# Kernel tuning notes

Measured on AMD Instinct MI355X. Metric: run time of the kernel, lower is better.

Reference implementation:

```python
import math
import jax, jax.numpy as jnp
import numpy as np

B, S, HID, H, NREL = 4, 512, 1024, 16, 64
D = HID // H  # per-head size = 64, must equal relation embedding dim


def setup_inputs() -> dict:
    key = jax.random.key(0)
    ks = jax.random.split(key, 12)
    w = lambda k, shape: jax.random.normal(k, shape, jnp.float32) * 0.02
    return {
        "q_in": jax.random.normal(ks[0], (B, S, HID), jnp.float32),
        "k_in": jax.random.normal(ks[1], (B, S, HID), jnp.float32),
        "v_in": jax.random.normal(ks[2], (B, S, HID), jnp.float32),
        "mask": jax.random.randint(ks[3], (B, 1, S, S), 0, NREL),
        "Wq": w(ks[4], (HID, HID)), "bq": jnp.zeros((HID,), jnp.float32),
        "Wk": w(ks[5], (HID, HID)), "bk": jnp.zeros((HID,), jnp.float32),
        "Wv": w(ks[6], (HID, HID)), "bv": jnp.zeros((HID,), jnp.float32),
        "Wo": w(ks[7], (HID, HID)), "bo": jnp.zeros((HID,), jnp.float32),
        "rel_k_table": w(ks[8], (NREL, D)),
        "rel_v_table": w(ks[9], (NREL, D)),
    }


def reference(q_in, k_in, v_in, mask, Wq, bq, Wk, bk, Wv, bv, Wo, bo,
              rel_k_table, rel_v_table):
    def proj(x, W, b):  # [B,S,HID] -> [B,H,S,D]
        return (x @ W.T + b).reshape(B, S, H, D).transpose(0, 2, 1, 3)

    q = proj(q_in, Wq, bq)
    k = proj(k_in, Wk, bk)
    v = proj(v_in, Wv, bv)

    ids = mask[:, 0]                      # [B,S,S] relation ids
    rel_k = rel_k_table[ids]              # [B,S,S,D]
    rel_v = rel_v_table[ids]              # [B,S,S,D]

    scores = jnp.einsum('bhqd,bhkd->bhqk', q, k)
    scores = scores + jnp.einsum('bhqd,bqkd->bhqk', q, rel_k) / 4.0
    scores = scores / math.sqrt(float(D))

    bias = (1.0 - (mask > 0).astype(scores.dtype)) * -10000.0  # [B,1,S,S]
    probs = jax.nn.softmax(scores + bias, axis=-1)             # [B,H,S,S]

    out = jnp.einsum('bhqk,bhkd->bhqd', probs, v)
    out = out + 0.25 * jnp.einsum('bhqk,bqkd->bhqd', probs, rel_v)
    out = out.transpose(0, 2, 1, 3).reshape(B, S, HID)
    return out @ Wo.T + bo
```

## Files before the change

kernel.cpp:

```cpp
#include <hip/hip_runtime.h>


typedef __attribute__((ext_vector_type(8))) short bf16x8 __attribute__((may_alias));
typedef __attribute__((ext_vector_type(4))) float f32x4;

__device__ __forceinline__ short f2bf(float x) {
    unsigned u = __float_as_uint(x);
    u += 0x7fff + ((u >> 16) & 1);
    return (short)(u >> 16);
}

__device__ __forceinline__ void async16(void* lds, const void* g) {
    __builtin_amdgcn_global_load_lds(
        (const __attribute__((address_space(1))) void*)g,
        (__attribute__((address_space(3))) void*)lds, 16, 0, 0);
}

__global__ __launch_bounds__(256)
void cast_all(const float* __restrict__ x0, const float* __restrict__ x1, const float* __restrict__ x2,
              const float* __restrict__ w0, const float* __restrict__ w1,
              const float* __restrict__ w2, const float* __restrict__ w3,
              short* __restrict__ y0, short* __restrict__ y1, short* __restrict__ y2,
              short* __restrict__ u0, short* __restrict__ u1,
              short* __restrict__ u2, short* __restrict__ u3)
{
    size_t i = (size_t)blockIdx.x * 256 + threadIdx.x;
    const float* src; short* dst; size_t off;
    if (i < 3u*524288u) {
        int s = (int)(i / 524288u); off = i % 524288u;
        src = s == 0 ? x0 : (s == 1 ? x1 : x2);
        dst = s == 0 ? y0 : (s == 1 ? y1 : y2);
    } else {
        size_t j = i - 3u*524288u;
        int s = (int)(j / 262144u); off = j % 262144u;
        src = s == 0 ? w0 : (s == 1 ? w1 : (s == 2 ? w2 : w3));
        dst = s == 0 ? u0 : (s == 1 ? u1 : (s == 2 ? u2 : u3));
    }
    float4 f = ((const float4*)src)[off];
    short4 o; o.x = f2bf(f.x); o.y = f2bf(f.y); o.z = f2bf(f.z); o.w = f2bf(f.w);
    ((short4*)dst)[off] = o;
}

__global__ __launch_bounds__(256)
void gemm_bf16(const short* __restrict__ A0, const short* __restrict__ A1, const short* __restrict__ A2,
               const short* __restrict__ B0, const short* __restrict__ B1, const short* __restrict__ B2,
               const float* __restrict__ c0, const float* __restrict__ c1, const float* __restrict__ c2,
               void* __restrict__ O0, void* __restrict__ O1, void* __restrict__ O2,
               int mode)
{
    __shared__ short ldsw[128 * 64 + 64 * 64];
    short* Als = ldsw;
    short* Bls = ldsw + 128 * 64;

    const int z = blockIdx.z;
    const short* A    = z == 0 ? A0 : (z == 1 ? A1 : A2);
    const short* Bm   = z == 0 ? B0 : (z == 1 ? B1 : B2);
    const float* bias = z == 0 ? c0 : (z == 1 ? c1 : c2);
    void*        O    = z == 0 ? O0 : (z == 1 ? O1 : O2);

    const int t = threadIdx.x;
    const int lane = t & 63, w = t >> 6;
    const int rowBase = blockIdx.y * 128;
    const int colBase = blockIdx.x * 64;
    const int gl = ((lane & 7) - (lane >> 3)) & 7;

    f32x4 acc[2][4];
#pragma unroll
    for (int i = 0; i < 2; ++i)
#pragma unroll
        for (int j = 0; j < 4; ++j) acc[i][j] = (f32x4){0.f, 0.f, 0.f, 0.f};

    const int rstage = w * 8 + (lane >> 3);
    const short* Ag = A  + (size_t)(rowBase + rstage) * 1024 + gl * 8;
    const short* Bg = Bm + (size_t)(colBase + rstage) * 1024 + gl * 8;

    for (int it = 0; it < 16; ++it) {
        const int k0 = it * 64;
#pragma unroll
        for (int i = 0; i < 4; ++i)
            async16(&Als[(i * 32 + w * 8) * 64], Ag + (size_t)i * 32 * 1024 + k0);
#pragma unroll
        for (int i = 0; i < 2; ++i)
            async16(&Bls[(i * 32 + w * 8) * 64], Bg + (size_t)i * 32 * 1024 + k0);
        __syncthreads();
#pragma unroll
        for (int kk = 0; kk < 2; ++kk) {
            bf16x8 a[2], b[4];
#pragma unroll
            for (int mi = 0; mi < 2; ++mi) {
                int r = w * 32 + mi * 16 + (lane & 15);
                int s = (kk * 4 + (lane >> 4) + r) & 7;
                a[mi] = *(const bf16x8*)&Als[r * 64 + s * 8];
            }
#pragma unroll
            for (int ni = 0; ni < 4; ++ni) {
                int r = ni * 16 + (lane & 15);
                int s = (kk * 4 + (lane >> 4) + r) & 7;
                b[ni] = *(const bf16x8*)&Bls[r * 64 + s * 8];
            }
#pragma unroll
            for (int mi = 0; mi < 2; ++mi)
#pragma unroll
                for (int ni = 0; ni < 4; ++ni)
                    acc[mi][ni] = __builtin_amdgcn_mfma_f32_16x16x32_bf16(
                        a[mi], b[ni], acc[mi][ni], 0, 0, 0);
        }
        __syncthreads();
    }

    const int quad = lane >> 4, cl = lane & 15;
    if (mode == 1 && z == 2) {
        short* Tls = ldsw;
#pragma unroll
        for (int mi = 0; mi < 2; ++mi)
#pragma unroll
            for (int ni = 0; ni < 4; ++ni) {
                int d = ni * 16 + cl;
                float bv = bias[colBase + d];
                short4 pk;
                pk.x = f2bf(acc[mi][ni][0] + bv);
                pk.y = f2bf(acc[mi][ni][1] + bv);
                pk.z = f2bf(acc[mi][ni][2] + bv);
                pk.w = f2bf(acc[mi][ni][3] + bv);
                int sl = w * 32 + mi * 16 + quad * 4;
                *(short4*)&Tls[d * 136 + sl] = pk;
            }
        __syncthreads();
        int d = t >> 2, s0 = (t & 3) * 32;
        int bb = rowBase >> 9, hh = colBase >> 6, sBase = rowBase & 511;
        short* dst = (short*)O + (((size_t)(bb * 16 + hh) * 64 + d) << 9) + sBase + s0;
#pragma unroll
        for (int j = 0; j < 4; ++j)
            *(bf16x8*)(dst + j * 8) = *(const bf16x8*)&Tls[d * 136 + s0 + j * 8];
        return;
    }

#pragma unroll
    for (int mi = 0; mi < 2; ++mi) {
#pragma unroll
        for (int ni = 0; ni < 4; ++ni) {
            int col = colBase + ni * 16 + cl;
            float bv = bias[col];
#pragma unroll
            for (int reg = 0; reg < 4; ++reg) {
                int row = rowBase + w * 32 + mi * 16 + quad * 4 + reg;
                float val = acc[mi][ni][reg] + bv;
                if (mode == 1) {
                    int bb = row >> 9, s = row & 511;
                    int hh = col >> 6, d = col & 63;
                    ((short*)O)[(((size_t)(bb * 16 + hh) * 512 + s) << 6) + d] = f2bf(val);
                } else {
                    ((float*)O)[(size_t)row * 1024 + col] = val;
                }
            }
        }
    }
}

#define A_LDS_BINS 4160
#define A_LDS_OPP  21568
#define A_LDS_LP   38208
#define A_LDS_INV  38464
#define A_LDS_TOT  38528

__global__ __launch_bounds__(256)
void attn_kernel(const short* __restrict__ qg, const short* __restrict__ kg,
                 const short* __restrict__ vtg, const int* __restrict__ mask,
                 const float* __restrict__ relk, const float* __restrict__ relv,
                 short* __restrict__ attn_b)
{
    __shared__ __align__(16) char pool[A_LDS_TOT];
    float* qwr    = (float*)pool;
    short* binsBf = (short*)pool;
    float* binsA  = (float*)(pool + A_LDS_BINS);
    float* Lp     = (float*)(pool + A_LDS_LP);
    float* invl   = (float*)(pool + A_LDS_INV);

    const int t = threadIdx.x, lane = t & 63, w = t >> 6;
    const int quad = lane >> 4, cl = lane & 15;
    const int bid = blockIdx.x, qbk = bid & 31, bh = bid >> 5;
    const int b = bh >> 4, h = bh & 15, q0 = qbk * 16;

    const short* qbase = qg  + ((size_t)bh * 512 + q0) * 64;
    const short* kbase = kg  + (size_t)bh * 512 * 64;
    const short* vbase = vtg + (size_t)bh * 64 * 512;
    const int*   mb    = mask + (size_t)b * 512 * 512 + (size_t)q0 * 512;

    float* bins_w = binsA + w * (16 * 68);
    short* Pst    = (short*)(pool + A_LDS_OPP + w * 4160);
    float* Op_w   = (float*)(pool + A_LDS_OPP + w * 4160);

    for (int i = t; i < 4 * 16 * 68; i += 256) binsA[i] = 0.f;

    bf16x8 rvb0, rvb1;
    {
        const float* rp = relv + (size_t)(quad * 8) * 64 + w * 16 + cl;
#pragma unroll
        for (int j = 0; j < 8; ++j) rvb0[j] = f2bf(rp[j * 64]);
#pragma unroll
        for (int j = 0; j < 8; ++j) rvb1[j] = f2bf(rp[2048 + j * 64]);
    }

    bf16x8 qa0 = *(const bf16x8*)(qbase + cl * 64 + quad * 8);
    bf16x8 qa1 = *(const bf16x8*)(qbase + cl * 64 + 32 + quad * 8);

    {
        const float* kp = relk + (size_t)(w * 16 + cl) * 64 + quad * 8;
        bf16x8 rb0, rb1;
#pragma unroll
        for (int j = 0; j < 8; ++j) rb0[j] = f2bf(kp[j]);
#pragma unroll
        for (int j = 0; j < 8; ++j) rb1[j] = f2bf(kp[32 + j]);
        f32x4 qr = (f32x4){0.f, 0.f, 0.f, 0.f};
        qr = __builtin_amdgcn_mfma_f32_16x16x32_bf16(qa0, rb0, qr, 0, 0, 0);
        qr = __builtin_amdgcn_mfma_f32_16x16x32_bf16(qa1, rb1, qr, 0, 0, 0);
#pragma unroll
        for (int reg = 0; reg < 4; ++reg)
            qwr[(quad * 4 + reg) * 65 + w * 16 + cl] = qr[reg];
    }
    __syncthreads();

    f32x4 oacc[4];
#pragma unroll
    for (int dt = 0; dt < 4; ++dt) oacc[dt] = (f32x4){0.f, 0.f, 0.f, 0.f};
    float lpart[4] = {0.f, 0.f, 0.f, 0.f};

#pragma unroll
    for (int c = 0; c < 2; ++c) {
        const int k0 = w * 128 + c * 64;
#pragma unroll
        for (int nt = 0; nt < 4; ++nt) {
            const short* kp = kbase + (size_t)(k0 + nt * 16 + cl) * 64 + quad * 8;
            bf16x8 kb0 = *(const bf16x8*)kp;
            bf16x8 kb1 = *(const bf16x8*)(kp + 32);
            f32x4 s = (f32x4){0.f, 0.f, 0.f, 0.f};
            s = __builtin_amdgcn_mfma_f32_16x16x32_bf16(qa0, kb0, s, 0, 0, 0);
            s = __builtin_amdgcn_mfma_f32_16x16x32_bf16(qa1, kb1, s, 0, 0, 0);
            const int kidx = k0 + nt * 16 + cl;
#pragma unroll
            for (int reg = 0; reg < 4; ++reg) {
                int q = quad * 4 + reg;
                int id = mb[q * 512 + kidx];
                float sc = (s[reg] + 0.25f * qwr[q * 65 + id]) * 0.125f;
                sc = (id == 0) ? sc - 10000.f : sc;
                float p = __expf(sc);
                lpart[reg] += p;
                atomicAdd(&bins_w[q * 68 + id], p);
                Pst[q * 72 + nt * 16 + cl] = f2bf(p);
            }
        }
        bf16x8 pa0 = *(const bf16x8*)&Pst[cl * 72 + quad * 8];
        bf16x8 pa1 = *(const bf16x8*)&Pst[cl * 72 + 32 + quad * 8];
#pragma unroll
        for (int dt = 0; dt < 4; ++dt) {
            const short* vp = vbase + (size_t)(dt * 16 + cl) * 512 + k0 + quad * 8;
            bf16x8 vb0 = *(const bf16x8*)vp;
            bf16x8 vb1 = *(const bf16x8*)(vp + 32);
            oacc[dt] = __builtin_amdgcn_mfma_f32_16x16x32_bf16(pa0, vb0, oacc[dt], 0, 0, 0);
            oacc[dt] = __builtin_amdgcn_mfma_f32_16x16x32_bf16(pa1, vb1, oacc[dt], 0, 0, 0);
        }
    }

#pragma unroll
    for (int reg = 0; reg < 4; ++reg) {
        int q = quad * 4 + reg;
#pragma unroll
        for (int dt = 0; dt < 4; ++dt)
            Op_w[q * 65 + dt * 16 + cl] = oacc[dt][reg];
        float lsum = lpart[reg];
#pragma unroll
        for (int m = 8; m >= 1; m >>= 1) lsum += __shfl_xor(lsum, m);
        if (cl == 0) Lp[w * 16 + q] = lsum;
    }
    __syncthreads();

    if (t < 16)
        invl[t] = 1.0f / (Lp[t] + Lp[16 + t] + Lp[32 + t] + Lp[48 + t]);
    {
        int q = t >> 4, r0 = (t & 15) * 4;
        float4 s0 = *(const float4*)&binsA[0 * 1088 + q * 68 + r0];
        float4 s1 = *(const float4*)&binsA[1 * 1088 + q * 68 + r0];
        float4 s2 = *(const float4*)&binsA[2 * 1088 + q * 68 + r0];
        float4 s3 = *(const float4*)&binsA[3 * 1088 + q * 68 + r0];
        short4 o;
        o.x = f2bf(s0.x + s1.x + s2.x + s3.x);
        o.y = f2bf(s0.y + s1.y + s2.y + s3.y);
        o.z = f2bf(s0.z + s1.z + s2.z + s3.z);
        o.w = f2bf(s0.w + s1.w + s2.w + s3.w);
        *(short4*)&binsBf[q * 72 + r0] = o;
    }
    __syncthreads();

    bf16x8 ba0 = *(const bf16x8*)&binsBf[cl * 72 + quad * 8];
    bf16x8 ba1 = *(const bf16x8*)&binsBf[cl * 72 + 32 + quad * 8];
    f32x4 racc = (f32x4){0.f, 0.f, 0.f, 0.f};
    racc = __builtin_amdgcn_mfma_f32_16x16x32_bf16(ba0, rvb0, racc, 0, 0, 0);
    racc = __builtin_amdgcn_mfma_f32_16x16x32_bf16(ba1, rvb1, racc, 0, 0, 0);

#pragma unroll
    for (int reg = 0; reg < 4; ++reg) {
        int q = quad * 4 + reg;
        int d = w * 16 + cl;
        float osum = 0.f;
#pragma unroll
        for (int wv = 0; wv < 4; ++wv)
            osum += ((const float*)(pool + A_LDS_OPP + wv * 4160))[q * 65 + d];
        float val = (osum + 0.25f * racc[reg]) * invl[q];
        attn_b[(size_t)(b * 512 + q0 + q) * 1024 + h * 64 + d] = f2bf(val);
    }
}

extern "C" void kernel_launch(void* const* d_in, const int* in_sizes, int n_in,
                              void* d_out, int out_size, void* d_ws, size_t ws_size,
                              hipStream_t stream)
{
    const float* q_in = (const float*)d_in[0];
    const float* k_in = (const float*)d_in[1];
    const float* v_in = (const float*)d_in[2];
    const int*   mask = (const int*)d_in[3];
    const float* Wq   = (const float*)d_in[4];
    const float* bq   = (const float*)d_in[5];
    const float* Wk   = (const float*)d_in[6];
    const float* bk   = (const float*)d_in[7];
    const float* Wv   = (const float*)d_in[8];
    const float* bv   = (const float*)d_in[9];
    const float* Wo   = (const float*)d_in[10];
    const float* bo   = (const float*)d_in[11];
    const float* relk = (const float*)d_in[12];
    const float* relv = (const float*)d_in[13];

    char* ws = (char*)d_ws;
    short* qb     = (short*)(ws);
    short* kb     = (short*)(ws + (4u  << 20));
    short* vt     = (short*)(ws + (8u  << 20));
    short* attn_b = (short*)(ws + (12u << 20));
    short* Xq     = (short*)(ws + (16u << 20));
    short* Xk     = (short*)(ws + (20u << 20));
    short* Xv     = (short*)(ws + (24u << 20));
    short* Wqb    = (short*)(ws + (28u << 20));
    short* Wkb    = (short*)(ws + (30u << 20));
    short* Wvb    = (short*)(ws + (32u << 20));
    short* Wob    = (short*)(ws + (34u << 20));

    cast_all<<<10240, 256, 0, stream>>>(q_in, k_in, v_in, Wq, Wk, Wv, Wo,
                                        Xq, Xk, Xv, Wqb, Wkb, Wvb, Wob);

    gemm_bf16<<<dim3(16, 16, 3), 256, 0, stream>>>(
        Xq, Xk, Xv, Wqb, Wkb, Wvb, bq, bk, bv, qb, kb, vt, 1);

    attn_kernel<<<dim3(2048), 256, 0, stream>>>(qb, kb, vt, mask, relk, relv, attn_b);

    gemm_bf16<<<dim3(16, 16, 1), 256, 0, stream>>>(
        attn_b, attn_b, attn_b, Wob, Wob, Wob, bo, bo, bo,
        (void*)d_out, (void*)d_out, (void*)d_out, 0);
}
```

Baseline: 243.7 us.

## Widen GEMM tiles to 128x128, stage epilogues via LDS, shrink attention LDS

The projection and output GEMMs move from 128x64 to 128x128 tiles with a 2x2 wave layout, doubling per-wave MFMA work and reuse. The Q/K epilogue now goes through LDS so head-major stores are vectorized. The attention kernel replaces per-wave bins and partial-output buffers with shared atomically accumulated buffers, cutting LDS roughly in half to allow more resident blocks (launch bounds set to 6). It also preloads mask ids ahead of the score loop. The trade-offs are more LDS atomic contention in attention and fewer GEMM blocks (128 for the output projection) on a large GPU.

After: 300.7 us. 23.4% more time.

```diff
diff --git a/kernel.cpp b/kernel.cpp
--- a/kernel.cpp
+++ b/kernel.cpp
@@ -42,13 +42,13 @@
 }
 
 __global__ __launch_bounds__(256)
-void gemm_bf16(const short* __restrict__ A0, const short* __restrict__ A1, const short* __restrict__ A2,
-               const short* __restrict__ B0, const short* __restrict__ B1, const short* __restrict__ B2,
-               const float* __restrict__ c0, const float* __restrict__ c1, const float* __restrict__ c2,
-               void* __restrict__ O0, void* __restrict__ O1, void* __restrict__ O2,
-               int mode)
+void gemm128(const short* __restrict__ A0, const short* __restrict__ A1, const short* __restrict__ A2,
+             const short* __restrict__ B0, const short* __restrict__ B1, const short* __restrict__ B2,
+             const float* __restrict__ c0, const float* __restrict__ c1, const float* __restrict__ c2,
+             void* __restrict__ O0, void* __restrict__ O1, void* __restrict__ O2,
+             int mode)
 {
-    __shared__ short ldsw[128 * 64 + 64 * 64];
+    __shared__ short ldsw[128 * 136];
     short* Als = ldsw;
     short* Bls = ldsw + 128 * 64;
 
@@ -60,13 +60,15 @@
 
     const int t = threadIdx.x;
     const int lane = t & 63, w = t >> 6;
+    const int wr = w >> 1, wc = w & 1;
+    const int quad = lane >> 4, cl = lane & 15;
     const int rowBase = blockIdx.y * 128;
-    const int colBase = blockIdx.x * 64;
+    const int colBase = blockIdx.x * 128;
     const int gl = ((lane & 7) - (lane >> 3)) & 7;
 
-    f32x4 acc[2][4];
-#pragma unroll
-    for (int i = 0; i < 2; ++i)
+    f32x4 acc[4][4];
+#pragma unroll
+    for (int i = 0; i < 4; ++i)
 #pragma unroll
         for (int j = 0; j < 4; ++j) acc[i][j] = (f32x4){0.f, 0.f, 0.f, 0.f};
 
@@ -80,26 +82,26 @@
         for (int i = 0; i < 4; ++i)
             async16(&Als[(i * 32 + w * 8) * 64], Ag + (size_t)i * 32 * 1024 + k0);
 #pragma unroll
-        for (int i = 0; i < 2; ++i)
+        for (int i = 0; i < 4; ++i)
             async16(&Bls[(i * 32 + w * 8) * 64], Bg + (size_t)i * 32 * 1024 + k0);
         __syncthreads();
 #pragma unroll
         for (int kk = 0; kk < 2; ++kk) {
-            bf16x8 a[2], b[4];
-#pragma unroll
-            for (int mi = 0; mi < 2; ++mi) {
-                int r = w * 32 + mi * 16 + (lane & 15);
-                int s = (kk * 4 + (lane >> 4) + r) & 7;
+            bf16x8 a[4], b[4];
+#pragma unroll
+            for (int mi = 0; mi < 4; ++mi) {
+                int r = wr * 64 + mi * 16 + cl;
+                int s = (kk * 4 + quad + r) & 7;
                 a[mi] = *(const bf16x8*)&Als[r * 64 + s * 8];
             }
 #pragma unroll
             for (int ni = 0; ni < 4; ++ni) {
-                int r = ni * 16 + (lane & 15);
-                int s = (kk * 4 + (lane >> 4) + r) & 7;
+                int r = wc * 64 + ni * 16 + cl;
+                int s = (kk * 4 + quad + r) & 7;
                 b[ni] = *(const bf16x8*)&Bls[r * 64 + s * 8];
             }
 #pragma unroll
-            for (int mi = 0; mi < 2; ++mi)
+            for (int mi = 0; mi < 4; ++mi)
 #pragma unroll
                 for (int ni = 0; ni < 4; ++ni)
                     acc[mi][ni] = __builtin_amdgcn_mfma_f32_16x16x32_bf16(
@@ -108,62 +110,79 @@
         __syncthreads();
     }
 
-    const int quad = lane >> 4, cl = lane & 15;
-    if (mode == 1 && z == 2) {
-        short* Tls = ldsw;
-#pragma unroll
-        for (int mi = 0; mi < 2; ++mi)
+    if (mode == 0) {
+#pragma unroll
+        for (int mi = 0; mi < 4; ++mi)
 #pragma unroll
             for (int ni = 0; ni < 4; ++ni) {
-                int d = ni * 16 + cl;
+                int col = colBase + wc * 64 + ni * 16 + cl;
+                float bv = bias[col];
+#pragma unroll
+                for (int reg = 0; reg < 4; ++reg) {
+                    int row = rowBase + wr * 64 + mi * 16 + quad * 4 + reg;
+                    ((float*)O)[(size_t)row * 1024 + col] = acc[mi][ni][reg] + bv;
+                }
+            }
+        return;
+    }
+
+    short* Tls = ldsw;
+    if (z == 2) {
+#pragma unroll
+        for (int mi = 0; mi < 4; ++mi)
+#pragma unroll
+            for (int ni = 0; ni < 4; ++ni) {
+                int d = wc * 64 + ni * 16 + cl;
                 float bv = bias[colBase + d];
                 short4 pk;
                 pk.x = f2bf(acc[mi][ni][0] + bv);
                 pk.y = f2bf(acc[mi][ni][1] + bv);
                 pk.z = f2bf(acc[mi][ni][2] + bv);
                 pk.w = f2bf(acc[mi][ni][3] + bv);
-                int sl = w * 32 + mi * 16 + quad * 4;
+                int sl = wr * 64 + mi * 16 + quad * 4;
                 *(short4*)&Tls[d * 136 + sl] = pk;
             }
         __syncthreads();
-        int d = t >> 2, s0 = (t & 3) * 32;
-        int bb = rowBase >> 9, hh = colBase >> 6, sBase = rowBase & 511;
-        short* dst = (short*)O + (((size_t)(bb * 16 + hh) * 64 + d) << 9) + sBase + s0;
-#pragma unroll
-        for (int j = 0; j < 4; ++j)
-            *(bf16x8*)(dst + j * 8) = *(const bf16x8*)&Tls[d * 136 + s0 + j * 8];
-        return;
-    }
-
-#pragma unroll
-    for (int mi = 0; mi < 2; ++mi) {
-#pragma unroll
-        for (int ni = 0; ni < 4; ++ni) {
-            int col = colBase + ni * 16 + cl;
-            float bv = bias[col];
-#pragma unroll
-            for (int reg = 0; reg < 4; ++reg) {
-                int row = rowBase + w * 32 + mi * 16 + quad * 4 + reg;
-                float val = acc[mi][ni][reg] + bv;
-                if (mode == 1) {
-                    int bb = row >> 9, s = row & 511;
-                    int hh = col >> 6, d = col & 63;
-                    ((short*)O)[(((size_t)(bb * 16 + hh) * 512 + s) << 6) + d] = f2bf(val);
-                } else {
-                    ((float*)O)[(size_t)row * 1024 + col] = val;
+        int dl = t >> 4, sl8 = (t & 15) * 8;
+        int bb = rowBase >> 9, sBase = rowBase & 511, hh0 = colBase >> 6;
+#pragma unroll
+        for (int dd = 0; dd < 8; ++dd) {
+            int d_local = dd * 16 + dl;
+            int hh = hh0 + (d_local >> 6), d = d_local & 63;
+            short* dst = (short*)O + (((size_t)(bb * 16 + hh) * 64 + d) << 9) + sBase + sl8;
+            *(bf16x8*)dst = *(const bf16x8*)&Tls[d_local * 136 + sl8];
+        }
+    } else {
+#pragma unroll
+        for (int mi = 0; mi < 4; ++mi)
+#pragma unroll
+            for (int ni = 0; ni < 4; ++ni) {
+                int d = wc * 64 + ni * 16 + cl;
+                float bv = bias[colBase + d];
+#pragma unroll
+                for (int reg = 0; reg < 4; ++reg) {
+                    int sl = wr * 64 + mi * 16 + quad * 4 + reg;
+                    Tls[sl * 136 + d] = f2bf(acc[mi][ni][reg] + bv);
                 }
             }
-        }
-    }
-}
-
-#define A_LDS_BINS 4160
-#define A_LDS_OPP  21568
-#define A_LDS_LP   38208
-#define A_LDS_INV  38464
-#define A_LDS_TOT  38528
-
-__global__ __launch_bounds__(256)
+        __syncthreads();
+        int sl = t >> 1, half = t & 1;
+        int bb = rowBase >> 9, sBase = rowBase & 511, hh = (colBase >> 6) + half;
+        short* dst = (short*)O + (((size_t)(bb * 16 + hh) * 512 + sBase + sl) << 6);
+#pragma unroll
+        for (int j = 0; j < 8; ++j)
+            *(bf16x8*)(dst + j * 8) = *(const bf16x8*)&Tls[sl * 136 + half * 64 + j * 8];
+    }
+}
+
+#define A_OFF_BINS 4352
+#define A_OFF_OACC 8704
+#define A_OFF_LACC 13056
+#define A_OFF_INVL 13120
+#define A_OFF_PST  13184
+#define A_LDS_TOT  22400
+
+__global__ __launch_bounds__(256, 6)
 void attn_kernel(const short* __restrict__ qg, const short* __restrict__ kg,
                  const short* __restrict__ vtg, const int* __restrict__ mask,
                  const float* __restrict__ relk, const float* __restrict__ relv,
@@ -172,9 +191,10 @@
     __shared__ __align__(16) char pool[A_LDS_TOT];
     float* qwr    = (float*)pool;
     short* binsBf = (short*)pool;
-    float* binsA  = (float*)(pool + A_LDS_BINS);
-    float* Lp     = (float*)(pool + A_LDS_LP);
-    float* invl   = (float*)(pool + A_LDS_INV);
+    float* bins   = (float*)(pool + A_OFF_BINS);
+    float* Oacc   = (float*)(pool + A_OFF_OACC);
+    float* Lacc   = (float*)(pool + A_OFF_LACC);
+    float* invl   = (float*)(pool + A_OFF_INVL);
 
     const int t = threadIdx.x, lane = t & 63, w = t >> 6;
     const int quad = lane >> 4, cl = lane & 15;
@@ -186,11 +206,10 @@
     const short* vbase = vtg + (size_t)bh * 64 * 512;
     const int*   mb    = mask + (size_t)b * 512 * 512 + (size_t)q0 * 512;
 
-    float* bins_w = binsA + w * (16 * 68);
-    short* Pst    = (short*)(pool + A_LDS_OPP + w * 4160);
-    float* Op_w   = (float*)(pool + A_LDS_OPP + w * 4160);
-
-    for (int i = t; i < 4 * 16 * 68; i += 256) binsA[i] = 0.f;
+    short* Pst = (short*)(pool + A_OFF_PST + w * 2304);
+
+    for (int i = t; i < (A_OFF_PST - A_OFF_BINS) / 4; i += 256)
+        bins[i] = 0.f;
 
     bf16x8 rvb0, rvb1;
     {
@@ -216,7 +235,7 @@
         qr = __builtin_amdgcn_mfma_f32_16x16x32_bf16(qa1, rb1, qr, 0, 0, 0);
 #pragma unroll
         for (int reg = 0; reg < 4; ++reg)
-            qwr[(quad * 4 + reg) * 65 + w * 16 + cl] = qr[reg];
+            qwr[(quad * 4 + reg) * 68 + w * 16 + cl] = qr[reg];
     }
     __syncthreads();
 
@@ -228,6 +247,13 @@
 #pragma unroll
     for (int c = 0; c < 2; ++c) {
         const int k0 = w * 128 + c * 64;
+        int idv[4][4];
+#pragma unroll
+        for (int nt = 0; nt < 4; ++nt)
+#pragma unroll
+            for (int reg = 0; reg < 4; ++reg)
+                idv[nt][reg] = mb[(quad * 4 + reg) * 512 + k0 + nt * 16 + cl];
+
 #pragma unroll
         for (int nt = 0; nt < 4; ++nt) {
             const short* kp = kbase + (size_t)(k0 + nt * 16 + cl) * 64 + quad * 8;
@@ -236,16 +262,15 @@
             f32x4 s = (f32x4){0.f, 0.f, 0.f, 0.f};
             s = __builtin_amdgcn_mfma_f32_16x16x32_bf16(qa0, kb0, s, 0, 0, 0);
             s = __builtin_amdgcn_mfma_f32_16x16x32_bf16(qa1, kb1, s, 0, 0, 0);
-            const int kidx = k0 + nt * 16 + cl;
 #pragma unroll
             for (int reg = 0; reg < 4; ++reg) {
                 int q = quad * 4 + reg;
-                int id = mb[q * 512 + kidx];
-                float sc = (s[reg] + 0.25f * qwr[q * 65 + id]) * 0.125f;
+                int id = idv[nt][reg];
+                float sc = (s[reg] + 0.25f * qwr[q * 68 + id]) * 0.125f;
                 sc = (id == 0) ? sc - 10000.f : sc;
                 float p = __expf(sc);
                 lpart[reg] += p;
-                atomicAdd(&bins_w[q * 68 + id], p);
+                atomicAdd(&bins[q * 68 + id], p);
                 Pst[q * 72 + nt * 16 + cl] = f2bf(p);
             }
         }
@@ -266,27 +291,20 @@
         int q = quad * 4 + reg;
 #pragma unroll
         for (int dt = 0; dt < 4; ++dt)
-            Op_w[q * 65 + dt * 16 + cl] = oacc[dt][reg];
+            atomicAdd(&Oacc[q * 68 + dt * 16 + cl], oacc[dt][reg]);
         float lsum = lpart[reg];
 #pragma unroll
         for (int m = 8; m >= 1; m >>= 1) lsum += __shfl_xor(lsum, m);
-        if (cl == 0) Lp[w * 16 + q] = lsum;
+        if (cl == 0) atomicAdd(&Lacc[q], lsum);
     }
     __syncthreads();
 
-    if (t < 16)
-        invl[t] = 1.0f / (Lp[t] + Lp[16 + t] + Lp[32 + t] + Lp[48 + t]);
+    if (t < 16) invl[t] = 1.0f / Lacc[t];
     {
         int q = t >> 4, r0 = (t & 15) * 4;
-        float4 s0 = *(const float4*)&binsA[0 * 1088 + q * 68 + r0];
-        float4 s1 = *(const float4*)&binsA[1 * 1088 + q * 68 + r0];
-        float4 s2 = *(const float4*)&binsA[2 * 1088 + q * 68 + r0];
-        float4 s3 = *(const float4*)&binsA[3 * 1088 + q * 68 + r0];
+        float4 f = *(const float4*)&bins[q * 68 + r0];
         short4 o;
-        o.x = f2bf(s0.x + s1.x + s2.x + s3.x);
-        o.y = f2bf(s0.y + s1.y + s2.y + s3.y);
-        o.z = f2bf(s0.z + s1.z + s2.z + s3.z);
-        o.w = f2bf(s0.w + s1.w + s2.w + s3.w);
+        o.x = f2bf(f.x); o.y = f2bf(f.y); o.z = f2bf(f.z); o.w = f2bf(f.w);
         *(short4*)&binsBf[q * 72 + r0] = o;
     }
     __syncthreads();
@@ -301,11 +319,7 @@
     for (int reg = 0; reg < 4; ++reg) {
         int q = quad * 4 + reg;
         int d = w * 16 + cl;
-        float osum = 0.f;
-#pragma unroll
-        for (int wv = 0; wv < 4; ++wv)
-            osum += ((const float*)(pool + A_LDS_OPP + wv * 4160))[q * 65 + d];
-        float val = (osum + 0.25f * racc[reg]) * invl[q];
+        float val = (Oacc[q * 68 + d] + 0.25f * racc[reg]) * invl[q];
         attn_b[(size_t)(b * 512 + q0 + q) * 1024 + h * 64 + d] = f2bf(val);
     }
 }
@@ -345,12 +359,12 @@
     cast_all<<<10240, 256, 0, stream>>>(q_in, k_in, v_in, Wq, Wk, Wv, Wo,
                                         Xq, Xk, Xv, Wqb, Wkb, Wvb, Wob);
 
-    gemm_bf16<<<dim3(16, 16, 3), 256, 0, stream>>>(
+    gemm128<<<dim3(8, 16, 3), 256, 0, stream>>>(
         Xq, Xk, Xv, Wqb, Wkb, Wvb, bq, bk, bv, qb, kb, vt, 1);
 
     attn_kernel<<<dim3(2048), 256, 0, stream>>>(qb, kb, vt, mask, relk, relv, attn_b);
 
-    gemm_bf16<<<dim3(16, 16, 1), 256, 0, stream>>>(
+    gemm128<<<dim3(8, 16, 1), 256, 0, stream>>>(
         attn_b, attn_b, attn_b, Wob, Wob, Wob, bo, bo, bo,
         (void*)d_out, (void*)d_out, (void*)d_out, 0);
 }
```
